# Kernel tuning notes

Hardware: AMD Instinct MI355X
Metric: run time of the kernel (lower is better)

The kernel has to match this reference:

```python
import jax, jax.numpy as jnp
import numpy as np

N_NODES = 100000
N_EDGES = 1600000
N_GRAPHS = 512
IN_DIM = 128
HID = 128
EDGE_DIM = 16
BN_EPS = 1e-5


def _gine_conv(x, edge_index, edge_attr, le_w, le_b, W1, b1, gamma, beta, W2, b2):
    # GINEConv (eps=0): out = MLP(x + sum_j ReLU(x_j + Lin(edge_attr_j)))
    src, dst = edge_index[0], edge_index[1]
    e = edge_attr @ le_w + le_b                      # [E, F]
    msg = jax.nn.relu(x[src] + e)                    # gather + add + relu
    agg = jax.ops.segment_sum(msg, dst, num_segments=N_NODES)
    h = agg + x                                      # (1+eps)*x, eps=0
    h = h @ W1 + b1
    mean = jnp.mean(h, axis=0)
    var = jnp.var(h, axis=0)
    h = (h - mean) * jax.lax.rsqrt(var + BN_EPS) * gamma + beta  # BatchNorm1d (batch stats)
    h = jax.nn.relu(h)
    return h @ W2 + b2


def setup_inputs() -> dict:
    key = jax.random.key(0)
    ks = jax.random.split(key, 20)
    s = 0.02
    inp = {
        'x': jax.random.normal(ks[0], (N_NODES, IN_DIM), jnp.float32),
        'edge_index': jax.random.randint(ks[1], (2, N_EDGES), 0, N_NODES, jnp.int32),
        'edge_attr': jax.random.normal(ks[2], (N_EDGES, EDGE_DIM), jnp.float32),
        'batch': jnp.sort(jax.random.randint(ks[3], (N_NODES,), 0, N_GRAPHS, jnp.int32)),
        # conv1 params
        'le1_w': jax.random.normal(ks[4], (EDGE_DIM, IN_DIM), jnp.float32) * s,
        'le1_b': jnp.zeros((IN_DIM,), jnp.float32),
        'W11': jax.random.normal(ks[5], (IN_DIM, HID), jnp.float32) * s,
        'b11': jnp.zeros((HID,), jnp.float32),
        'g1': jnp.ones((HID,), jnp.float32),
        'bt1': jnp.zeros((HID,), jnp.float32),
        'W12': jax.random.normal(ks[6], (HID, HID), jnp.float32) * s,
        'b12': jnp.zeros((HID,), jnp.float32),
        # conv2 params
        'le2_w': jax.random.normal(ks[7], (EDGE_DIM, HID), jnp.float32) * s,
        'le2_b': jnp.zeros((HID,), jnp.float32),
        'W21': jax.random.normal(ks[8], (HID, HID), jnp.float32) * s,
        'b21': jnp.zeros((HID,), jnp.float32),
        'g2': jnp.ones((HID,), jnp.float32),
        'bt2': jnp.zeros((HID,), jnp.float32),
        'W22': jax.random.normal(ks[9], (HID, HID), jnp.float32) * s,
        'b22': jnp.zeros((HID,), jnp.float32),
        # classifier
        'Wc1': jax.random.normal(ks[10], (HID, 64), jnp.float32) * s,
        'bc1': jnp.zeros((64,), jnp.float32),
        'Wc2': jax.random.normal(ks[11], (64, 2), jnp.float32) * s,
        'bc2': jnp.zeros((2,), jnp.float32),
    }
    return inp


def reference(x, edge_index, edge_attr, batch,
              le1_w, le1_b, W11, b11, g1, bt1, W12, b12,
              le2_w, le2_b, W21, b21, g2, bt2, W22, b22,
              Wc1, bc1, Wc2, bc2):
    h = jax.nn.relu(_gine_conv(x, edge_index, edge_attr, le1_w, le1_b, W11, b11, g1, bt1, W12, b12))
    h = jax.nn.relu(_gine_conv(h, edge_index, edge_attr, le2_w, le2_b, W21, b21, g2, bt2, W22, b22))
    pooled = jax.ops.segment_sum(h, batch, num_segments=N_GRAPHS)  # global_add_pool
    h = jax.nn.relu(pooled @ Wc1 + bc1)
    # Dropout(0.5) treated as identity (eval-mode reference)
    return h @ Wc2 + bc2
```

## Files before the change

kernel.cpp:

```cpp
#include <hip/hip_runtime.h>
#include <hip/hip_fp16.h>

#define N_NODES  100000
#define N_EDGES  1600000
#define N_GRAPHS 512
#define DIM      128
#define EDGE_DIM 16
#define BN_EPS   1e-5f
#define NGB      3125

typedef _Float16 h2 __attribute__((ext_vector_type(2)));

#if defined(__has_builtin)
#if __has_builtin(__builtin_amdgcn_fdot2)
#define HAVE_FDOT2 1
#endif
#endif


__global__ __launch_bounds__(256) void k_hist(const int* __restrict__ dst,
                                              int* __restrict__ deg) {
    int e = blockIdx.x * 256 + threadIdx.x;
    if (e < N_EDGES) atomicAdd(&deg[dst[e]], 1);
}

__global__ __launch_bounds__(256) void k_scan1(const int* __restrict__ deg,
                                               int* __restrict__ rowptr1,
                                               int* __restrict__ sums, int N) {
    __shared__ int sc[256];
    int t = threadIdx.x;
    int base = blockIdx.x * 1024 + t * 4;
    int v0 = (base + 0 < N) ? deg[base + 0] : 0;
    int v1 = (base + 1 < N) ? deg[base + 1] : 0;
    int v2 = (base + 2 < N) ? deg[base + 2] : 0;
    int v3 = (base + 3 < N) ? deg[base + 3] : 0;
    v1 += v0; v2 += v1; v3 += v2;
    sc[t] = v3;
    __syncthreads();
    for (int o = 1; o < 256; o <<= 1) {
        int add = (t >= o) ? sc[t - o] : 0;
        __syncthreads();
        sc[t] += add;
        __syncthreads();
    }
    int prefix = sc[t] - v3;
    if (base + 0 < N) rowptr1[base + 0] = v0 + prefix;
    if (base + 1 < N) rowptr1[base + 1] = v1 + prefix;
    if (base + 2 < N) rowptr1[base + 2] = v2 + prefix;
    if (base + 3 < N) rowptr1[base + 3] = v3 + prefix;
    if (t == 255) sums[blockIdx.x] = sc[255];
}

__global__ __launch_bounds__(256) void k_scan2(int* __restrict__ sums, int n) {
    __shared__ int sc[256];
    int t = threadIdx.x;
    int v = (t < n) ? sums[t] : 0;
    sc[t] = v;
    __syncthreads();
    for (int o = 1; o < 256; o <<= 1) {
        int add = (t >= o) ? sc[t - o] : 0;
        __syncthreads();
        sc[t] += add;
        __syncthreads();
    }
    if (t < n) sums[t] = sc[t];
}

__global__ __launch_bounds__(256) void k_scan3(int* __restrict__ rowptr,
                                               int* __restrict__ cursor,
                                               const int* __restrict__ sums, int N) {
    int c = blockIdx.x;
    int off = (c == 0) ? 0 : sums[c - 1];
    int t = threadIdx.x;
    int base = c * 1024 + t * 4;
#pragma unroll
    for (int i = 0; i < 4; i++) {
        int g = base + i;
        if (g < N) {
            int val = rowptr[1 + g] + off;
            rowptr[1 + g] = val;
            if (g + 1 < N) cursor[g + 1] = val;
        }
    }
    if (c == 0 && t == 0) { rowptr[0] = 0; cursor[0] = 0; }
}

__global__ __launch_bounds__(256) void k_fill(const int* __restrict__ src,
                                              const int* __restrict__ dst,
                                              const float* __restrict__ edge_attr,
                                              int* __restrict__ cursor,
                                              int* __restrict__ csr_src,
                                              uint4* __restrict__ csr_ea) {
    int e = blockIdx.x * 256 + threadIdx.x;
    if (e < N_EDGES) {
        int d = dst[e];
        int p = atomicAdd(&cursor[d], 1);
        csr_src[p] = src[e];
        const float4* ea = (const float4*)(edge_attr + (size_t)e * EDGE_DIM);
        float4 a0 = ea[0], a1 = ea[1], a2 = ea[2], a3 = ea[3];
        union { __half h[16]; uint4 q[2]; } u;
        u.h[0]  = __float2half(a0.x); u.h[1]  = __float2half(a0.y);
        u.h[2]  = __float2half(a0.z); u.h[3]  = __float2half(a0.w);
        u.h[4]  = __float2half(a1.x); u.h[5]  = __float2half(a1.y);
        u.h[6]  = __float2half(a1.z); u.h[7]  = __float2half(a1.w);
        u.h[8]  = __float2half(a2.x); u.h[9]  = __float2half(a2.y);
        u.h[10] = __float2half(a2.z); u.h[11] = __float2half(a2.w);
        u.h[12] = __float2half(a3.x); u.h[13] = __float2half(a3.y);
        u.h[14] = __float2half(a3.z); u.h[15] = __float2half(a3.w);
        uint4* o = csr_ea + (size_t)p * 2;
        o[0] = u.q[0]; o[1] = u.q[1];
    }
}

union EaU { uint4 q[2]; h2 p[8]; };

__device__ __forceinline__ void edge_acc(float2 xr, uint4 q0, uint4 q1,
                                         const h2* wl0p, const h2* wl1p,
                                         float b0, float b1,
                                         float& acc0, float& acc1) {
    EaU u; u.q[0] = q0; u.q[1] = q1;
    float e0 = b0, e1 = b1;
#if HAVE_FDOT2
#pragma unroll
    for (int j = 0; j < 8; j++) {
        e0 = __builtin_amdgcn_fdot2(u.p[j], wl0p[j], e0, false);
        e1 = __builtin_amdgcn_fdot2(u.p[j], wl1p[j], e1, false);
    }
#else
#pragma unroll
    for (int j = 0; j < 8; j++) {
        float ax = (float)u.p[j].x, ay = (float)u.p[j].y;
        e0 = fmaf(ax, (float)wl0p[j].x, fmaf(ay, (float)wl0p[j].y, e0));
        e1 = fmaf(ax, (float)wl1p[j].x, fmaf(ay, (float)wl1p[j].y, e1));
    }
#endif
    acc0 += fmaxf(xr.x + e0, 0.f);
    acc1 += fmaxf(xr.y + e1, 0.f);
}

__global__ __launch_bounds__(256) void k_gine_msg(const float* __restrict__ x,
                                                  const uint4* __restrict__ csr_ea,
                                                  const int* __restrict__ rowptr,
                                                  const int* __restrict__ csr_src,
                                                  const float* __restrict__ lew,
                                                  const float* __restrict__ leb,
                                                  float* __restrict__ agg) {
    int lane = threadIdx.x & 63;
    int node = blockIdx.x * 4 + (threadIdx.x >> 6);
    int f0 = lane * 2;

    h2 wl0p[8], wl1p[8];
#pragma unroll
    for (int j = 0; j < 8; j++) {
        h2 a, b;
        a.x = (_Float16)lew[(2 * j + 0) * DIM + f0];
        a.y = (_Float16)lew[(2 * j + 1) * DIM + f0];
        b.x = (_Float16)lew[(2 * j + 0) * DIM + f0 + 1];
        b.y = (_Float16)lew[(2 * j + 1) * DIM + f0 + 1];
        wl0p[j] = a; wl1p[j] = b;
    }
    float b0 = leb[f0], b1 = leb[f0 + 1];

    float2 xv = *(const float2*)(x + (size_t)node * DIM + f0);
    float acc0 = xv.x, acc1 = xv.y;

    int pbeg = __builtin_amdgcn_readfirstlane(rowptr[node]);
    int pend = __builtin_amdgcn_readfirstlane(rowptr[node + 1]);

    int p = pbeg;
    for (; p + 4 <= pend; p += 4) {
        int s0 = __builtin_amdgcn_readfirstlane(csr_src[p + 0]);
        int s1 = __builtin_amdgcn_readfirstlane(csr_src[p + 1]);
        int s2 = __builtin_amdgcn_readfirstlane(csr_src[p + 2]);
        int s3 = __builtin_amdgcn_readfirstlane(csr_src[p + 3]);

        const uint4* ea = csr_ea + (size_t)p * 2;
        uint4 a00 = ea[0], a01 = ea[1];
        uint4 a10 = ea[2], a11 = ea[3];
        uint4 a20 = ea[4], a21 = ea[5];
        uint4 a30 = ea[6], a31 = ea[7];

        float2 x0 = *(const float2*)(x + (size_t)s0 * DIM + f0);
        float2 x1 = *(const float2*)(x + (size_t)s1 * DIM + f0);
        float2 x2 = *(const float2*)(x + (size_t)s2 * DIM + f0);
        float2 x3 = *(const float2*)(x + (size_t)s3 * DIM + f0);

        edge_acc(x0, a00, a01, wl0p, wl1p, b0, b1, acc0, acc1);
        edge_acc(x1, a10, a11, wl0p, wl1p, b0, b1, acc0, acc1);
        edge_acc(x2, a20, a21, wl0p, wl1p, b0, b1, acc0, acc1);
        edge_acc(x3, a30, a31, wl0p, wl1p, b0, b1, acc0, acc1);
    }
    for (; p < pend; p++) {
        int s0 = __builtin_amdgcn_readfirstlane(csr_src[p]);
        const uint4* ea = csr_ea + (size_t)p * 2;
        uint4 a0 = ea[0], a1 = ea[1];
        float2 x0 = *(const float2*)(x + (size_t)s0 * DIM + f0);
        edge_acc(x0, a0, a1, wl0p, wl1p, b0, b1, acc0, acc1);
    }

    float2 o; o.x = acc0; o.y = acc1;
    *(float2*)(agg + (size_t)node * DIM + f0) = o;
}

template <int MODE>
__global__ __launch_bounds__(256) void k_gemm(const float* __restrict__ A,
                                              const float* __restrict__ W,
                                              const float* __restrict__ bias,
                                              const float* __restrict__ colstat,
                                              float* __restrict__ part,
                                              const float* __restrict__ gamma,
                                              const float* __restrict__ beta,
                                              const int* __restrict__ batch,
                                              float* __restrict__ pooled,
                                              float* __restrict__ out, int M) {
    __shared__ float As[32][DIM];
    __shared__ float cA[DIM], cB[DIM];
    int t = threadIdx.x;
    int rbase = blockIdx.x * 32;

    if (MODE != 0) {
        if (t < DIM) {
            float inv_n = 1.f / (float)N_NODES;
            float mean = colstat[t] * inv_n;
            float var = colstat[DIM + t] * inv_n - mean * mean;
            float a = gamma[t] * rsqrtf(var + BN_EPS);
            cA[t] = a;
            cB[t] = beta[t] - mean * a;
        }
        __syncthreads();
    }

#pragma unroll
    for (int i = 0; i < 16; i++) {
        int idx = t + i * 256;
        int r = idx >> 7, c = idx & 127;
        int gr = rbase + r;
        float v = (gr < M) ? A[(size_t)gr * DIM + c] : 0.f;
        if (MODE != 0) {
            v = cA[c] * v + cB[c];
            v = v > 0.f ? v : 0.f;
        }
        As[r][c] = v;
    }
    __syncthreads();

    int cq = (t & 31) * 4;
    int rg = (t >> 5) * 4;
    float acc[4][4] = {{0.f}};

    for (int k = 0; k < DIM; k++) {
        float4 w = *(const float4*)&W[(size_t)k * DIM + cq];
        float a0 = As[rg + 0][k], a1 = As[rg + 1][k];
        float a2 = As[rg + 2][k], a3 = As[rg + 3][k];
        acc[0][0] += a0 * w.x; acc[0][1] += a0 * w.y; acc[0][2] += a0 * w.z; acc[0][3] += a0 * w.w;
        acc[1][0] += a1 * w.x; acc[1][1] += a1 * w.y; acc[1][2] += a1 * w.z; acc[1][3] += a1 * w.w;
        acc[2][0] += a2 * w.x; acc[2][1] += a2 * w.y; acc[2][2] += a2 * w.z; acc[2][3] += a2 * w.w;
        acc[3][0] += a3 * w.x; acc[3][1] += a3 * w.y; acc[3][2] += a3 * w.z; acc[3][3] += a3 * w.w;
    }

    float4 bb = *(const float4*)&bias[cq];
    float o[4][4];
#pragma unroll
    for (int i = 0; i < 4; i++) {
        o[i][0] = acc[i][0] + bb.x;
        o[i][1] = acc[i][1] + bb.y;
        o[i][2] = acc[i][2] + bb.z;
        o[i][3] = acc[i][3] + bb.w;
        if (MODE != 0) {
#pragma unroll
            for (int j = 0; j < 4; j++) o[i][j] = o[i][j] > 0.f ? o[i][j] : 0.f;
        }
    }

    if (MODE != 2) {
#pragma unroll
        for (int i = 0; i < 4; i++) {
            int gr = rbase + rg + i;
            if (gr < M) {
                float4 v; v.x = o[i][0]; v.y = o[i][1]; v.z = o[i][2]; v.w = o[i][3];
                *(float4*)&out[(size_t)gr * DIM + cq] = v;
            }
        }
    }

    if (MODE == 0) {
        float s[4] = {0.f, 0.f, 0.f, 0.f}, q[4] = {0.f, 0.f, 0.f, 0.f};
#pragma unroll
        for (int i = 0; i < 4; i++) {
            int gr = rbase + rg + i;
            if (gr < M) {
#pragma unroll
                for (int j = 0; j < 4; j++) {
                    s[j] += o[i][j];
                    q[j] += o[i][j] * o[i][j];
                }
            }
        }
        __syncthreads();
        float* s1 = &As[0][0];
        float* s2 = &As[8][0];
        int rgi = t >> 5;
#pragma unroll
        for (int j = 0; j < 4; j++) {
            s1[rgi * DIM + cq + j] = s[j];
            s2[rgi * DIM + cq + j] = q[j];
        }
        __syncthreads();
        float* srcp = (t < DIM) ? s1 : s2;
        int col = t & 127;
        float ts = 0.f;
#pragma unroll
        for (int k = 0; k < 8; k++) ts += srcp[k * DIM + col];
        part[(size_t)blockIdx.x * 256 + t] = ts;
    }

    if (MODE == 2) {
        int gr0 = rbase + rg;
        int b0 = (gr0 + 0 < M) ? batch[gr0 + 0] : -1;
        int b3 = (gr0 + 3 < M) ? batch[gr0 + 3] : -1;
        if (b0 == b3 && b0 >= 0) {
#pragma unroll
            for (int j = 0; j < 4; j++) {
                float v = o[0][j] + o[1][j] + o[2][j] + o[3][j];
                atomicAdd(&pooled[(size_t)b0 * DIM + cq + j], v);
            }
        } else {
            int bs[4];
            bs[0] = b0;
            bs[1] = (gr0 + 1 < M) ? batch[gr0 + 1] : -1;
            bs[2] = (gr0 + 2 < M) ? batch[gr0 + 2] : -1;
            bs[3] = b3;
#pragma unroll
            for (int i = 0; i < 4; i++) {
                if (bs[i] >= 0) {
#pragma unroll
                    for (int j = 0; j < 4; j++)
                        atomicAdd(&pooled[(size_t)bs[i] * DIM + cq + j], o[i][j]);
                }
            }
        }
    }
}

__global__ __launch_bounds__(256) void k_redstats(const float* __restrict__ part,
                                                  float* __restrict__ colstat) {
    int t = threadIdx.x;
    float s = 0.f;
    for (int r = blockIdx.x; r < NGB; r += gridDim.x)
        s += part[(size_t)r * 256 + t];
    atomicAdd(&colstat[t], s);
}

__global__ __launch_bounds__(64) void k_cls(const float* __restrict__ pooled,
                                            const float* __restrict__ Wc1,
                                            const float* __restrict__ bc1,
                                            const float* __restrict__ Wc2,
                                            const float* __restrict__ bc2,
                                            float* __restrict__ out) {
    __shared__ float row[DIM];
    __shared__ float t1[64];
    int g = blockIdx.x, t = threadIdx.x;
    row[t] = pooled[g * DIM + t];
    row[64 + t] = pooled[g * DIM + 64 + t];
    __syncthreads();
    float acc = bc1[t];
    for (int k = 0; k < DIM; k++) acc += row[k] * Wc1[k * 64 + t];
    t1[t] = acc > 0.f ? acc : 0.f;
    __syncthreads();
    if (t < 2) {
        float o = bc2[t];
        for (int j = 0; j < 64; j++) o += t1[j] * Wc2[j * 2 + t];
        out[g * 2 + t] = o;
    }
}


extern "C" void kernel_launch(void* const* d_in, const int* in_sizes, int n_in,
                              void* d_out, int out_size, void* d_ws, size_t ws_size,
                              hipStream_t stream) {
    const float* x          = (const float*)d_in[0];
    const int*   edge_index = (const int*)d_in[1];
    const float* edge_attr  = (const float*)d_in[2];
    const int*   batch      = (const int*)d_in[3];
    const float* le1_w = (const float*)d_in[4];
    const float* le1_b = (const float*)d_in[5];
    const float* W11   = (const float*)d_in[6];
    const float* b11   = (const float*)d_in[7];
    const float* g1    = (const float*)d_in[8];
    const float* bt1   = (const float*)d_in[9];
    const float* W12   = (const float*)d_in[10];
    const float* b12   = (const float*)d_in[11];
    const float* le2_w = (const float*)d_in[12];
    const float* le2_b = (const float*)d_in[13];
    const float* W21   = (const float*)d_in[14];
    const float* b21   = (const float*)d_in[15];
    const float* g2    = (const float*)d_in[16];
    const float* bt2   = (const float*)d_in[17];
    const float* W22   = (const float*)d_in[18];
    const float* b22   = (const float*)d_in[19];
    const float* Wc1   = (const float*)d_in[20];
    const float* bc1   = (const float*)d_in[21];
    const float* Wc2   = (const float*)d_in[22];
    const float* bc2   = (const float*)d_in[23];
    float* out = (float*)d_out;

    const int* srcp = edge_index;
    const int* dstp = edge_index + N_EDGES;

    char* ws = (char*)d_ws;
    size_t off = 0;
    auto carve = [&](size_t bytes) -> char* {
        char* p = ws + off;
        off += (bytes + 255) & ~(size_t)255;
        return p;
    };
    float* X0      = (float*)carve((size_t)N_NODES * DIM * 4);
    float* X1      = (float*)carve((size_t)N_NODES * DIM * 4);
    int*   rowptr  = (int*)carve((size_t)(N_NODES + 1) * 4);
    int*   cursor  = (int*)carve((size_t)N_NODES * 4);
    int*   sums    = (int*)carve(256 * 4);
    int*   csr_src = (int*)carve((size_t)N_EDGES * 4);
    uint4* csr_ea  = (uint4*)carve((size_t)N_EDGES * 32);
    float* part    = (float*)carve((size_t)NGB * 256 * 4);
    float* zreg    = (float*)carve((2 * DIM + 2 * DIM + (size_t)N_GRAPHS * DIM) * 4);
    float* colstat1 = zreg;
    float* colstat2 = zreg + 2 * DIM;
    float* pooled   = zreg + 4 * DIM;
    (void)ws_size; (void)in_sizes; (void)n_in; (void)out_size;

    const int nch = (N_NODES + 1023) / 1024;

    hipMemsetAsync(cursor, 0, (size_t)N_NODES * 4, stream);
    hipMemsetAsync(zreg, 0, (4 * DIM + (size_t)N_GRAPHS * DIM) * 4, stream);

    k_hist<<<(N_EDGES + 255) / 256, 256, 0, stream>>>(dstp, cursor);
    k_scan1<<<nch, 256, 0, stream>>>(cursor, rowptr + 1, sums, N_NODES);
    k_scan2<<<1, 256, 0, stream>>>(sums, nch);
    k_scan3<<<nch, 256, 0, stream>>>(rowptr, cursor, sums, N_NODES);
    k_fill<<<(N_EDGES + 255) / 256, 256, 0, stream>>>(srcp, dstp, edge_attr, cursor,
                                                      csr_src, csr_ea);

    k_gine_msg<<<N_NODES / 4, 256, 0, stream>>>(x, csr_ea, rowptr, csr_src, le1_w, le1_b, X0);
    k_gemm<0><<<NGB, 256, 0, stream>>>(X0, W11, b11, nullptr, part, nullptr, nullptr,
                                       nullptr, nullptr, X1, N_NODES);
    k_redstats<<<64, 256, 0, stream>>>(part, colstat1);
    k_gemm<1><<<NGB, 256, 0, stream>>>(X1, W12, b12, colstat1, nullptr, g1, bt1,
                                       nullptr, nullptr, X0, N_NODES);

    k_gine_msg<<<N_NODES / 4, 256, 0, stream>>>(X0, csr_ea, rowptr, csr_src, le2_w, le2_b, X1);
    k_gemm<0><<<NGB, 256, 0, stream>>>(X1, W21, b21, nullptr, part, nullptr, nullptr,
                                       nullptr, nullptr, X0, N_NODES);
    k_redstats<<<64, 256, 0, stream>>>(part, colstat2);
    k_gemm<2><<<NGB, 256, 0, stream>>>(X0, W22, b22, colstat2, nullptr, g2, bt2,
                                       batch, pooled, nullptr, N_NODES);

    k_cls<<<N_GRAPHS, 64, 0, stream>>>(pooled, Wc1, bc1, Wc2, bc2, out);
}
```

Before: 946.4 us.

## Gather node features in fp16 and unroll GEMM inner loop by four

Node features read by the edge-gather kernel are now stored as fp16: the input x goes through a new conversion kernel, and the second layer's MLP output is written directly in fp16. This halves the bytes per random gather, which is the dominant memory traffic in message passing. The GEMM inner loop is also unrolled by four with vectorized shared-memory reads, and the kernel gets an occupancy hint in its launch bounds. The cost is reduced precision in the gathered features and one extra conversion pass over x.

```diff
diff --git a/kernel.cpp b/kernel.cpp
--- a/kernel.cpp
+++ b/kernel.cpp
@@ -9,6 +9,7 @@
 #define BN_EPS   1e-5f
 #define NGB      3125
 
+typedef _Float16 f16;
 typedef _Float16 h2 __attribute__((ext_vector_type(2)));
 
 #if defined(__has_builtin)
@@ -98,23 +99,28 @@
         csr_src[p] = src[e];
         const float4* ea = (const float4*)(edge_attr + (size_t)e * EDGE_DIM);
         float4 a0 = ea[0], a1 = ea[1], a2 = ea[2], a3 = ea[3];
-        union { __half h[16]; uint4 q[2]; } u;
-        u.h[0]  = __float2half(a0.x); u.h[1]  = __float2half(a0.y);
-        u.h[2]  = __float2half(a0.z); u.h[3]  = __float2half(a0.w);
-        u.h[4]  = __float2half(a1.x); u.h[5]  = __float2half(a1.y);
-        u.h[6]  = __float2half(a1.z); u.h[7]  = __float2half(a1.w);
-        u.h[8]  = __float2half(a2.x); u.h[9]  = __float2half(a2.y);
-        u.h[10] = __float2half(a2.z); u.h[11] = __float2half(a2.w);
-        u.h[12] = __float2half(a3.x); u.h[13] = __float2half(a3.y);
-        u.h[14] = __float2half(a3.z); u.h[15] = __float2half(a3.w);
+        union { f16 h[16]; uint4 q[2]; } u;
+        u.h[0]  = (f16)a0.x; u.h[1]  = (f16)a0.y; u.h[2]  = (f16)a0.z; u.h[3]  = (f16)a0.w;
+        u.h[4]  = (f16)a1.x; u.h[5]  = (f16)a1.y; u.h[6]  = (f16)a1.z; u.h[7]  = (f16)a1.w;
+        u.h[8]  = (f16)a2.x; u.h[9]  = (f16)a2.y; u.h[10] = (f16)a2.z; u.h[11] = (f16)a2.w;
+        u.h[12] = (f16)a3.x; u.h[13] = (f16)a3.y; u.h[14] = (f16)a3.z; u.h[15] = (f16)a3.w;
         uint4* o = csr_ea + (size_t)p * 2;
         o[0] = u.q[0]; o[1] = u.q[1];
     }
 }
 
+__global__ __launch_bounds__(256) void k_cvt(const float* __restrict__ in,
+                                             f16* __restrict__ outh) {
+    size_t i = ((size_t)blockIdx.x * 256 + threadIdx.x) * 4;
+    float4 v = *(const float4*)(in + i);
+    union { f16 h[4]; uint2 u; } pk;
+    pk.h[0] = (f16)v.x; pk.h[1] = (f16)v.y; pk.h[2] = (f16)v.z; pk.h[3] = (f16)v.w;
+    *(uint2*)(outh + i) = pk.u;
+}
+
 union EaU { uint4 q[2]; h2 p[8]; };
 
-__device__ __forceinline__ void edge_acc(float2 xr, uint4 q0, uint4 q1,
+__device__ __forceinline__ void edge_acc(h2 xr, uint4 q0, uint4 q1,
                                          const h2* wl0p, const h2* wl1p,
                                          float b0, float b1,
                                          float& acc0, float& acc1) {
@@ -134,11 +140,11 @@
         e1 = fmaf(ax, (float)wl1p[j].x, fmaf(ay, (float)wl1p[j].y, e1));
     }
 #endif
-    acc0 += fmaxf(xr.x + e0, 0.f);
-    acc1 += fmaxf(xr.y + e1, 0.f);
-}
-
-__global__ __launch_bounds__(256) void k_gine_msg(const float* __restrict__ x,
+    acc0 += fmaxf((float)xr.x + e0, 0.f);
+    acc1 += fmaxf((float)xr.y + e1, 0.f);
+}
+
+__global__ __launch_bounds__(256) void k_gine_msg(const f16* __restrict__ xh,
                                                   const uint4* __restrict__ csr_ea,
                                                   const int* __restrict__ rowptr,
                                                   const int* __restrict__ csr_src,
@@ -153,16 +159,16 @@
 #pragma unroll
     for (int j = 0; j < 8; j++) {
         h2 a, b;
-        a.x = (_Float16)lew[(2 * j + 0) * DIM + f0];
-        a.y = (_Float16)lew[(2 * j + 1) * DIM + f0];
-        b.x = (_Float16)lew[(2 * j + 0) * DIM + f0 + 1];
-        b.y = (_Float16)lew[(2 * j + 1) * DIM + f0 + 1];
+        a.x = (f16)lew[(2 * j + 0) * DIM + f0];
+        a.y = (f16)lew[(2 * j + 1) * DIM + f0];
+        b.x = (f16)lew[(2 * j + 0) * DIM + f0 + 1];
+        b.y = (f16)lew[(2 * j + 1) * DIM + f0 + 1];
         wl0p[j] = a; wl1p[j] = b;
     }
     float b0 = leb[f0], b1 = leb[f0 + 1];
 
-    float2 xv = *(const float2*)(x + (size_t)node * DIM + f0);
-    float acc0 = xv.x, acc1 = xv.y;
+    h2 xv = *(const h2*)(xh + (size_t)node * DIM + f0);
+    float acc0 = (float)xv.x, acc1 = (float)xv.y;
 
     int pbeg = __builtin_amdgcn_readfirstlane(rowptr[node]);
     int pend = __builtin_amdgcn_readfirstlane(rowptr[node + 1]);
@@ -180,10 +186,10 @@
         uint4 a20 = ea[4], a21 = ea[5];
         uint4 a30 = ea[6], a31 = ea[7];
 
-        float2 x0 = *(const float2*)(x + (size_t)s0 * DIM + f0);
-        float2 x1 = *(const float2*)(x + (size_t)s1 * DIM + f0);
-        float2 x2 = *(const float2*)(x + (size_t)s2 * DIM + f0);
-        float2 x3 = *(const float2*)(x + (size_t)s3 * DIM + f0);
+        h2 x0 = *(const h2*)(xh + (size_t)s0 * DIM + f0);
+        h2 x1 = *(const h2*)(xh + (size_t)s1 * DIM + f0);
+        h2 x2 = *(const h2*)(xh + (size_t)s2 * DIM + f0);
+        h2 x3 = *(const h2*)(xh + (size_t)s3 * DIM + f0);
 
         edge_acc(x0, a00, a01, wl0p, wl1p, b0, b1, acc0, acc1);
         edge_acc(x1, a10, a11, wl0p, wl1p, b0, b1, acc0, acc1);
@@ -194,7 +200,7 @@
         int s0 = __builtin_amdgcn_readfirstlane(csr_src[p]);
         const uint4* ea = csr_ea + (size_t)p * 2;
         uint4 a0 = ea[0], a1 = ea[1];
-        float2 x0 = *(const float2*)(x + (size_t)s0 * DIM + f0);
+        h2 x0 = *(const h2*)(xh + (size_t)s0 * DIM + f0);
         edge_acc(x0, a0, a1, wl0p, wl1p, b0, b1, acc0, acc1);
     }
 
@@ -203,16 +209,17 @@
 }
 
 template <int MODE>
-__global__ __launch_bounds__(256) void k_gemm(const float* __restrict__ A,
-                                              const float* __restrict__ W,
-                                              const float* __restrict__ bias,
-                                              const float* __restrict__ colstat,
-                                              float* __restrict__ part,
-                                              const float* __restrict__ gamma,
-                                              const float* __restrict__ beta,
-                                              const int* __restrict__ batch,
-                                              float* __restrict__ pooled,
-                                              float* __restrict__ out, int M) {
+__global__ __launch_bounds__(256, 6) void k_gemm(const float* __restrict__ A,
+                                                 const float* __restrict__ W,
+                                                 const float* __restrict__ bias,
+                                                 const float* __restrict__ colstat,
+                                                 float* __restrict__ part,
+                                                 const float* __restrict__ gamma,
+                                                 const float* __restrict__ beta,
+                                                 const int* __restrict__ batch,
+                                                 float* __restrict__ pooled,
+                                                 float* __restrict__ out,
+                                                 f16* __restrict__ outh, int M) {
     __shared__ float As[32][DIM];
     __shared__ float cA[DIM], cB[DIM];
     int t = threadIdx.x;
@@ -248,14 +255,19 @@
     int rg = (t >> 5) * 4;
     float acc[4][4] = {{0.f}};
 
-    for (int k = 0; k < DIM; k++) {
-        float4 w = *(const float4*)&W[(size_t)k * DIM + cq];
-        float a0 = As[rg + 0][k], a1 = As[rg + 1][k];
-        float a2 = As[rg + 2][k], a3 = As[rg + 3][k];
-        acc[0][0] += a0 * w.x; acc[0][1] += a0 * w.y; acc[0][2] += a0 * w.z; acc[0][3] += a0 * w.w;
-        acc[1][0] += a1 * w.x; acc[1][1] += a1 * w.y; acc[1][2] += a1 * w.z; acc[1][3] += a1 * w.w;
-        acc[2][0] += a2 * w.x; acc[2][1] += a2 * w.y; acc[2][2] += a2 * w.z; acc[2][3] += a2 * w.w;
-        acc[3][0] += a3 * w.x; acc[3][1] += a3 * w.y; acc[3][2] += a3 * w.z; acc[3][3] += a3 * w.w;
+    for (int k4 = 0; k4 < DIM; k4 += 4) {
+        float4 w0 = *(const float4*)&W[(size_t)(k4 + 0) * DIM + cq];
+        float4 w1 = *(const float4*)&W[(size_t)(k4 + 1) * DIM + cq];
+        float4 w2 = *(const float4*)&W[(size_t)(k4 + 2) * DIM + cq];
+        float4 w3 = *(const float4*)&W[(size_t)(k4 + 3) * DIM + cq];
+#pragma unroll
+        for (int i = 0; i < 4; i++) {
+            float4 a = *(const float4*)&As[rg + i][k4];
+            acc[i][0] += a.x * w0.x + a.y * w1.x + a.z * w2.x + a.w * w3.x;
+            acc[i][1] += a.x * w0.y + a.y * w1.y + a.z * w2.y + a.w * w3.y;
+            acc[i][2] += a.x * w0.z + a.y * w1.z + a.z * w2.z + a.w * w3.z;
+            acc[i][3] += a.x * w0.w + a.y * w1.w + a.z * w2.w + a.w * w3.w;
+        }
     }
 
     float4 bb = *(const float4*)&bias[cq];
@@ -272,7 +284,7 @@
         }
     }
 
-    if (MODE != 2) {
+    if (MODE == 0) {
 #pragma unroll
         for (int i = 0; i < 4; i++) {
             int gr = rbase + rg + i;
@@ -281,9 +293,6 @@
                 *(float4*)&out[(size_t)gr * DIM + cq] = v;
             }
         }
-    }
-
-    if (MODE == 0) {
         float s[4] = {0.f, 0.f, 0.f, 0.f}, q[4] = {0.f, 0.f, 0.f, 0.f};
 #pragma unroll
         for (int i = 0; i < 4; i++) {
@@ -312,6 +321,19 @@
 #pragma unroll
         for (int k = 0; k < 8; k++) ts += srcp[k * DIM + col];
         part[(size_t)blockIdx.x * 256 + t] = ts;
+    }
+
+    if (MODE == 1) {
+#pragma unroll
+        for (int i = 0; i < 4; i++) {
+            int gr = rbase + rg + i;
+            if (gr < M) {
+                union { f16 h[4]; uint2 u; } pk;
+                pk.h[0] = (f16)o[i][0]; pk.h[1] = (f16)o[i][1];
+                pk.h[2] = (f16)o[i][2]; pk.h[3] = (f16)o[i][3];
+                *(uint2*)&outh[(size_t)gr * DIM + cq] = pk.u;
+            }
+        }
     }
 
     if (MODE == 2) {
@@ -414,8 +436,8 @@
         off += (bytes + 255) & ~(size_t)255;
         return p;
     };
-    float* X0      = (float*)carve((size_t)N_NODES * DIM * 4);
-    float* X1      = (float*)carve((size_t)N_NODES * DIM * 4);
+    float* A       = (float*)carve((size_t)N_NODES * DIM * 4);
+    float* B       = (float*)carve((size_t)N_NODES * DIM * 4);
     int*   rowptr  = (int*)carve((size_t)(N_NODES + 1) * 4);
     int*   cursor  = (int*)carve((size_t)N_NODES * 4);
     int*   sums    = (int*)carve(256 * 4);
@@ -428,11 +450,15 @@
     float* pooled   = zreg + 4 * DIM;
     (void)ws_size; (void)in_sizes; (void)n_in; (void)out_size;
 
+    f16* xh0 = (f16*)B;
+    f16* xh1 = (f16*)A;
+
     const int nch = (N_NODES + 1023) / 1024;
 
     hipMemsetAsync(cursor, 0, (size_t)N_NODES * 4, stream);
     hipMemsetAsync(zreg, 0, (4 * DIM + (size_t)N_GRAPHS * DIM) * 4, stream);
 
+    k_cvt<<<(N_NODES * DIM) / 1024, 256, 0, stream>>>(x, xh0);
     k_hist<<<(N_EDGES + 255) / 256, 256, 0, stream>>>(dstp, cursor);
     k_scan1<<<nch, 256, 0, stream>>>(cursor, rowptr + 1, sums, N_NODES);
     k_scan2<<<1, 256, 0, stream>>>(sums, nch);
@@ -440,19 +466,21 @@
     k_fill<<<(N_EDGES + 255) / 256, 256, 0, stream>>>(srcp, dstp, edge_attr, cursor,
                                                       csr_src, csr_ea);
 
-    k_gine_msg<<<N_NODES / 4, 256, 0, stream>>>(x, csr_ea, rowptr, csr_src, le1_w, le1_b, X0);
-    k_gemm<0><<<NGB, 256, 0, stream>>>(X0, W11, b11, nullptr, part, nullptr, nullptr,
-                                       nullptr, nullptr, X1, N_NODES);
+    k_gine_msg<<<N_NODES / 4, 256, 0, stream>>>(xh0, csr_ea, rowptr, csr_src,
+                                                le1_w, le1_b, A);
+    k_gemm<0><<<NGB, 256, 0, stream>>>(A, W11, b11, nullptr, part, nullptr, nullptr,
+                                       nullptr, nullptr, B, nullptr, N_NODES);
     k_redstats<<<64, 256, 0, stream>>>(part, colstat1);
-    k_gemm<1><<<NGB, 256, 0, stream>>>(X1, W12, b12, colstat1, nullptr, g1, bt1,
-                                       nullptr, nullptr, X0, N_NODES);
-
-    k_gine_msg<<<N_NODES / 4, 256, 0, stream>>>(X0, csr_ea, rowptr, csr_src, le2_w, le2_b, X1);
-    k_gemm<0><<<NGB, 256, 0, stream>>>(X1, W21, b21, nullptr, part, nullptr, nullptr,
-                                       nullptr, nullptr, X0, N_NODES);
+    k_gemm<1><<<NGB, 256, 0, stream>>>(B, W12, b12, colstat1, nullptr, g1, bt1,
+                                       nullptr, nullptr, nullptr, xh1, N_NODES);
+
+    k_gine_msg<<<N_NODES / 4, 256, 0, stream>>>(xh1, csr_ea, rowptr, csr_src,
+                                                le2_w, le2_b, B);
+    k_gemm<0><<<NGB, 256, 0, stream>>>(B, W21, b21, nullptr, part, nullptr, nullptr,
+                                       nullptr, nullptr, A, nullptr, N_NODES);
     k_redstats<<<64, 256, 0, stream>>>(part, colstat2);
-    k_gemm<2><<<NGB, 256, 0, stream>>>(X0, W22, b22, colstat2, nullptr, g2, bt2,
-                                       batch, pooled, nullptr, N_NODES);
+    k_gemm<2><<<NGB, 256, 0, stream>>>(A, W22, b22, colstat2, nullptr, g2, bt2,
+                                       batch, pooled, nullptr, nullptr, N_NODES);
 
     k_cls<<<N_GRAPHS, 64, 0, stream>>>(pooled, Wc1, bc1, Wc2, bc2, out);
 }
```

After: 964.5 us. About the same (+1.9%).
